# Optimization experiments

Hardware: AMD Instinct MI355X
Metric: run time of the kernel (lower is better)

The kernel has to match this reference:

```python
import jax, jax.numpy as jnp
import numpy as np

B, N_SRC, N_TGT = 2, 2048, 2048
DIM, HEADS, DIM_HEAD, DIM_ROT = 1024, 16, 64, 32
INNER = HEADS * DIM_HEAD
SCALE = DIM_HEAD ** -0.5


def rotate_every_two(x):
    # (..., d) with d even: pairs (x1, x2) -> (-x2, x1), interleaved
    x1 = x[..., ::2]
    x2 = x[..., 1::2]
    return jnp.stack((-x2, x1), axis=-1).reshape(x.shape)


def setup_inputs() -> dict:
    key = jax.random.key(0)
    ks = jax.random.split(key, 10)
    return {
        "src": jax.random.normal(ks[0], (B, N_SRC, DIM), jnp.float32),
        "sin_src": jax.random.uniform(ks[1], (B, N_SRC, DIM_ROT), jnp.float32, -1.0, 1.0),
        "cos_src": jax.random.uniform(ks[2], (B, N_SRC, DIM_ROT), jnp.float32, -1.0, 1.0),
        "tgt": jax.random.normal(ks[3], (B, N_TGT, DIM), jnp.float32),
        "sin_tgt": jax.random.uniform(ks[4], (B, N_TGT, DIM_ROT), jnp.float32, -1.0, 1.0),
        "cos_tgt": jax.random.uniform(ks[5], (B, N_TGT, DIM_ROT), jnp.float32, -1.0, 1.0),
        "wq": jax.random.normal(ks[6], (DIM, INNER), jnp.float32) / np.sqrt(DIM),
        "wkv": jax.random.normal(ks[7], (DIM, 2 * INNER), jnp.float32) / np.sqrt(DIM),
        "wout": jax.random.normal(ks[8], (INNER, DIM), jnp.float32) / np.sqrt(INNER),
        "bout": jnp.zeros((DIM,), jnp.float32),
    }


def reference(src, sin_src, cos_src, tgt, sin_tgt, cos_tgt, wq, wkv, wout, bout):
    b = src.shape[0]
    q = tgt @ wq                                  # (b, i, inner)
    k, v = jnp.split(src @ wkv, 2, axis=-1)       # (b, j, inner) each

    def split_heads(t):
        return t.reshape(b, t.shape[1], HEADS, DIM_HEAD).transpose(0, 2, 1, 3)

    q, k, v = map(split_heads, (q, k, v))          # (b, h, n, d)

    # rotary on leading DIM_ROT dims; pos embs broadcast across heads
    st, ct = sin_tgt[:, None], cos_tgt[:, None]    # (b, 1, i, dr)
    ss, cs = sin_src[:, None], cos_src[:, None]    # (b, 1, j, dr)
    q_rot, q_pass = q[..., :DIM_ROT], q[..., DIM_ROT:]
    k_rot, k_pass = k[..., :DIM_ROT], k[..., DIM_ROT:]
    q_rot = q_rot * ct + rotate_every_two(q_rot) * st
    k_rot = k_rot * cs + rotate_every_two(k_rot) * ss
    q = jnp.concatenate([q_rot, q_pass], axis=-1)
    k = jnp.concatenate([k_rot, k_pass], axis=-1)

    dots = jnp.einsum('bhid,bhjd->bhij', q, k) * SCALE
    attn = jax.nn.softmax(dots, axis=-1)
    out = jnp.einsum('bhij,bhjd->bhid', attn, v)
    out = out.transpose(0, 2, 1, 3).reshape(b, out.shape[2], INNER)
    return out @ wout + bout, attn
```

## Files before the change

### kernel.cpp

```cpp
#include <hip/hip_runtime.h>
#include <hip/hip_bf16.h>
#include <cstdint>
#include <cstddef>

#define NB 2
#define NSEQ 2048
#define NHEADS 16
#define HD 64
#define DMODEL 1024
#define SCALEF 0.125f

typedef __attribute__((ext_vector_type(4))) float f32x4;
typedef __attribute__((ext_vector_type(8))) short s16x8;

__device__ __forceinline__ unsigned short f2bf(float f) {
  union { float f; unsigned u; } v; v.f = f;
  unsigned u = v.u;
  return (unsigned short)((u + 0x7fffu + ((u >> 16) & 1u)) >> 16);
}

__global__ void k_convert(const float* __restrict__ in, unsigned short* __restrict__ out, int n4) {
  int i = blockIdx.x * blockDim.x + threadIdx.x;
  if (i >= n4) return;
  float4 v = ((const float4*)in)[i];
  ushort4 o;
  o.x = f2bf(v.x); o.y = f2bf(v.y); o.z = f2bf(v.z); o.w = f2bf(v.w);
  ((ushort4*)out)[i] = o;
}

__global__ void k_transpose(const float* __restrict__ w, unsigned short* __restrict__ wt, int K, int N) {
  __shared__ float t[64][65];
  int n0 = blockIdx.x * 64, k0 = blockIdx.y * 64;
  int c = threadIdx.x & 63, rb = threadIdx.x >> 6;
#pragma unroll
  for (int rr = 0; rr < 16; rr++) {
    int k = rb * 16 + rr;
    t[c][k] = w[(size_t)(k0 + k) * N + n0 + c];
  }
  __syncthreads();
#pragma unroll
  for (int rr = 0; rr < 16; rr++) {
    int n = rb * 16 + rr;
    wt[(size_t)(n0 + n) * K + k0 + c] = f2bf(t[n][c]);
  }
}

#define GLD16(gp, lp) __builtin_amdgcn_global_load_lds( \
    (const __attribute__((address_space(1))) unsigned int*)(gp), \
    (__attribute__((address_space(3))) unsigned int*)(lp), 16, 0, 0)

__global__ __launch_bounds__(256) void k_gemm(const unsigned short* __restrict__ A,
                                              const unsigned short* __restrict__ Bt,
                                              float* __restrict__ C,
                                              const float* __restrict__ bias,
                                              int M, int N, int K) {
  __shared__ unsigned short As[128 * 32];
  __shared__ unsigned short Bs[128 * 32];
  const int tid = threadIdx.x;
  const int lane = tid & 63, wid = tid >> 6;
  const int m0 = blockIdx.y * 128, n0 = blockIdx.x * 128;
  const int wr = wid >> 1, wc = wid & 1;
  const int lr = lane >> 2, l4 = lane & 3;
  const int lc = lane & 15, lg = lane >> 4;

  const unsigned short* pa0 = A + (size_t)(m0 + wid * 32 + lr) * K + l4 * 8;
  const unsigned short* pa1 = pa0 + (size_t)16 * K;
  const unsigned short* pb0 = Bt + (size_t)(n0 + wid * 32 + lr) * K + l4 * 8;
  const unsigned short* pb1 = pb0 + (size_t)16 * K;

  f32x4 acc[4][4] = {};

  for (int kt = 0; kt < K; kt += 32) {
    GLD16(pa0 + kt, &As[wid * 1024]);
    GLD16(pa1 + kt, &As[wid * 1024 + 512]);
    GLD16(pb0 + kt, &Bs[wid * 1024]);
    GLD16(pb1 + kt, &Bs[wid * 1024 + 512]);
    __syncthreads();
    s16x8 af[4], bfr[4];
#pragma unroll
    for (int m = 0; m < 4; m++)
      af[m] = *(const s16x8*)&As[(wr * 64 + m * 16 + lc) * 32 + lg * 8];
#pragma unroll
    for (int n = 0; n < 4; n++)
      bfr[n] = *(const s16x8*)&Bs[(wc * 64 + n * 16 + lc) * 32 + lg * 8];
    __builtin_amdgcn_s_setprio(1);
#pragma unroll
    for (int m = 0; m < 4; m++)
#pragma unroll
      for (int n = 0; n < 4; n++)
        acc[m][n] = __builtin_amdgcn_mfma_f32_16x16x32_bf16(af[m], bfr[n], acc[m][n], 0, 0, 0);
    __builtin_amdgcn_s_setprio(0);
    __syncthreads();
  }

  float bv[4] = {0.f, 0.f, 0.f, 0.f};
  if (bias) {
#pragma unroll
    for (int n = 0; n < 4; n++) bv[n] = bias[n0 + wc * 64 + n * 16 + lc];
  }
#pragma unroll
  for (int m = 0; m < 4; m++) {
#pragma unroll
    for (int n = 0; n < 4; n++) {
      int col = n0 + wc * 64 + n * 16 + lc;
#pragma unroll
      for (int r = 0; r < 4; r++) {
        int row = m0 + wr * 64 + m * 16 + lg * 4 + r;
        C[(size_t)row * N + col] = acc[m][n][r] + bv[n];
      }
    }
  }
}

__global__ void k_rope(const float* __restrict__ src, int row_stride,
                       const float* __restrict__ sinp, const float* __restrict__ cosp,
                       unsigned short* __restrict__ dst) {
  int tid = blockIdx.x * 256 + threadIdx.x;
  int p = tid & 31;
  int h = (tid >> 5) & 15;
  int i = (tid >> 9) & 2047;
  int b = tid >> 20;
  int d = p * 2;
  float2 x = *(const float2*)(src + (size_t)(b * NSEQ + i) * row_stride + h * HD + d);
  float o0, o1;
  if (p < 16) {
    size_t sc = (size_t)(b * NSEQ + i) * 32 + d;
    float2 cc = *(const float2*)(cosp + sc);
    float2 ss = *(const float2*)(sinp + sc);
    o0 = x.x * cc.x - x.y * ss.x;
    o1 = x.y * cc.y + x.x * ss.y;
  } else { o0 = x.x; o1 = x.y; }
  size_t off = ((size_t)(b * NHEADS + h) * NSEQ + i) * HD + d;
  unsigned pack = (unsigned)f2bf(o0) | ((unsigned)f2bf(o1) << 16);
  *(unsigned*)(dst + off) = pack;
}

__global__ void k_vtrans(const float* __restrict__ kv, unsigned short* __restrict__ vt) {
  __shared__ float t[64][65];
  int i0 = blockIdx.x * 64;
  int h = blockIdx.y, b = blockIdx.z;
  int c = threadIdx.x & 63, rb = threadIdx.x >> 6;
#pragma unroll
  for (int rr = 0; rr < 16; rr++) {
    int il = rb * 16 + rr;
    t[il][c] = kv[(size_t)(b * NSEQ + i0 + il) * 2048 + 1024 + h * HD + c];
  }
  __syncthreads();
#pragma unroll
  for (int rr = 0; rr < 16; rr++) {
    int dd = rb * 16 + rr;
    vt[((size_t)(b * NHEADS + h) * HD + dd) * NSEQ + i0 + c] = f2bf(t[c][dd]);
  }
}

#define SROWB 2056
__global__ __launch_bounds__(512, 4) void k_attn(const unsigned short* __restrict__ qh,
                                                 const unsigned short* __restrict__ kh,
                                                 const unsigned short* __restrict__ vt,
                                                 float* __restrict__ attn_g,
                                                 unsigned short* __restrict__ ctx) {
  __shared__ unsigned short Sbf[16 * SROWB];
  __shared__ float wred[8][16];
  __shared__ float rowmax_s[16];
  __shared__ float invr[16];
  float* part = (float*)Sbf;

  const int tid = threadIdx.x;
  const int lane = tid & 63, wid = tid >> 6;
  const int i0 = blockIdx.x * 16;
  const int h = blockIdx.y, b = blockIdx.z;
  const int lc = lane & 15, lg = lane >> 4;

  const unsigned short* qb = qh + ((size_t)(b * NHEADS + h) * NSEQ + i0) * HD;
  const unsigned short* kb = kh + (size_t)(b * NHEADS + h) * NSEQ * HD;
  const unsigned short* vb = vt + (size_t)(b * NHEADS + h) * HD * NSEQ;

  s16x8 aq0 = *(const s16x8*)&qb[lc * HD + lg * 8];
  s16x8 aq1 = *(const s16x8*)&qb[lc * HD + 32 + lg * 8];
  f32x4 sc[16];
  float mx[4] = {-1e30f, -1e30f, -1e30f, -1e30f};
#pragma unroll
  for (int jf = 0; jf < 16; jf++) {
    int j = wid * 256 + jf * 16;
    f32x4 acc = {};
    s16x8 bk0 = *(const s16x8*)&kb[(size_t)(j + lc) * HD + lg * 8];
    s16x8 bk1 = *(const s16x8*)&kb[(size_t)(j + lc) * HD + 32 + lg * 8];
    acc = __builtin_amdgcn_mfma_f32_16x16x32_bf16(aq0, bk0, acc, 0, 0, 0);
    acc = __builtin_amdgcn_mfma_f32_16x16x32_bf16(aq1, bk1, acc, 0, 0, 0);
#pragma unroll
    for (int r = 0; r < 4; r++) {
      float v = acc[r] * SCALEF;
      sc[jf][r] = v;
      mx[r] = fmaxf(mx[r], v);
    }
  }
#pragma unroll
  for (int off = 1; off <= 8; off <<= 1)
#pragma unroll
    for (int r = 0; r < 4; r++) mx[r] = fmaxf(mx[r], __shfl_xor(mx[r], off));
  if (lc == 0) {
#pragma unroll
    for (int r = 0; r < 4; r++) wred[wid][lg * 4 + r] = mx[r];
  }
  __syncthreads();
  if (tid < 16) {
    float m = -1e30f;
#pragma unroll
    for (int w = 0; w < 8; w++) m = fmaxf(m, wred[w][tid]);
    rowmax_s[tid] = m;
  }
  __syncthreads();

  float mrow[4], psum[4] = {0.f, 0.f, 0.f, 0.f};
#pragma unroll
  for (int r = 0; r < 4; r++) mrow[r] = rowmax_s[lg * 4 + r];
#pragma unroll
  for (int jf = 0; jf < 16; jf++) {
    int j = wid * 256 + jf * 16;
#pragma unroll
    for (int r = 0; r < 4; r++) {
      float e = __expf(sc[jf][r] - mrow[r]);
      sc[jf][r] = e;
      psum[r] += e;
      Sbf[(size_t)(lg * 4 + r) * SROWB + j + lc] = f2bf(e);
    }
  }
#pragma unroll
  for (int off = 1; off <= 8; off <<= 1)
#pragma unroll
    for (int r = 0; r < 4; r++) psum[r] += __shfl_xor(psum[r], off);
  if (lc == 0) {
#pragma unroll
    for (int r = 0; r < 4; r++) wred[wid][lg * 4 + r] = psum[r];
  }
  __syncthreads();
  if (tid < 16) {
    float s = 0.f;
#pragma unroll
    for (int w = 0; w < 8; w++) s += wred[w][tid];
    invr[tid] = 1.0f / s;
  }
  __syncthreads();

  float ivr[4];
#pragma unroll
  for (int r = 0; r < 4; r++) ivr[r] = invr[lg * 4 + r];
  {
    float* ab = attn_g + ((size_t)(b * NHEADS + h) * NSEQ + i0) * NSEQ + wid * 256 + lc;
#pragma unroll
    for (int jf = 0; jf < 16; jf++) {
#pragma unroll
      for (int r = 0; r < 4; r++)
        __builtin_nontemporal_store(sc[jf][r] * ivr[r],
                                    ab + (size_t)(lg * 4 + r) * NSEQ + jf * 16);
    }
  }

  f32x4 accd[4] = {};
#pragma unroll 2
  for (int jj = 0; jj < 8; jj++) {
    int jb = wid * 256 + jj * 32;
    s16x8 af = *(const s16x8*)&Sbf[(size_t)lc * SROWB + jb + lg * 8];
    __builtin_amdgcn_s_setprio(1);
#pragma unroll
    for (int f = 0; f < 4; f++) {
      s16x8 bv = *(const s16x8*)&vb[(size_t)(f * 16 + lc) * NSEQ + jb + lg * 8];
      accd[f] = __builtin_amdgcn_mfma_f32_16x16x32_bf16(af, bv, accd[f], 0, 0, 0);
    }
    __builtin_amdgcn_s_setprio(0);
  }
  __syncthreads();

  if (wid < 4) {
#pragma unroll
    for (int f = 0; f < 4; f++)
#pragma unroll
      for (int r = 0; r < 4; r++)
        part[((size_t)wid * 16 + lg * 4 + r) * 64 + f * 16 + lc] = accd[f][r];
  }
  __syncthreads();
  if (wid >= 4) {
#pragma unroll
    for (int f = 0; f < 4; f++)
#pragma unroll
      for (int r = 0; r < 4; r++)
        part[((size_t)(wid - 4) * 16 + lg * 4 + r) * 64 + f * 16 + lc] += accd[f][r];
  }
  __syncthreads();

  if (tid < 256) {
    const int oi = tid >> 4;
    const int d0 = (tid & 15) * 4;
    float4 p0 = *(float4*)&part[((size_t)0 * 16 + oi) * 64 + d0];
    float4 p1 = *(float4*)&part[((size_t)1 * 16 + oi) * 64 + d0];
    float4 p2 = *(float4*)&part[((size_t)2 * 16 + oi) * 64 + d0];
    float4 p3 = *(float4*)&part[((size_t)3 * 16 + oi) * 64 + d0];
    float iv = invr[oi];
    float4 tot;
    tot.x = (p0.x + p1.x + p2.x + p3.x) * iv;
    tot.y = (p0.y + p1.y + p2.y + p3.y) * iv;
    tot.z = (p0.z + p1.z + p2.z + p3.z) * iv;
    tot.w = (p0.w + p1.w + p2.w + p3.w) * iv;
    ushort4 o;
    o.x = f2bf(tot.x); o.y = f2bf(tot.y); o.z = f2bf(tot.z); o.w = f2bf(tot.w);
    *(ushort4*)&ctx[(size_t)(b * NSEQ + i0 + oi) * DMODEL + h * HD + d0] = o;
  }
}

extern "C" void kernel_launch(void* const* d_in, const int* in_sizes, int n_in,
                              void* d_out, int out_size, void* d_ws, size_t ws_size,
                              hipStream_t stream) {
  const float* src     = (const float*)d_in[0];
  const float* sin_src = (const float*)d_in[1];
  const float* cos_src = (const float*)d_in[2];
  const float* tgt     = (const float*)d_in[3];
  const float* sin_tgt = (const float*)d_in[4];
  const float* cos_tgt = (const float*)d_in[5];
  const float* wq      = (const float*)d_in[6];
  const float* wkv     = (const float*)d_in[7];
  const float* wout    = (const float*)d_in[8];
  const float* bout    = (const float*)d_in[9];

  if (ws_size < (size_t)109051904) return;

  uint8_t* w = (uint8_t*)d_ws;
  unsigned short* tgt_bf = (unsigned short*)(w + 0);
  unsigned short* src_bf = (unsigned short*)(w + 8388608);
  unsigned short* wq_t   = (unsigned short*)(w + 16777216);
  unsigned short* wkv_t  = (unsigned short*)(w + 18874368);
  unsigned short* wout_t = (unsigned short*)(w + 23068672);
  float*          q_ws   = (float*)(w + 25165824);
  float*          kv_ws  = (float*)(w + 41943040);
  unsigned short* qhb    = (unsigned short*)(w + 75497472);
  unsigned short* khb    = (unsigned short*)(w + 83886080);
  unsigned short* vtb    = (unsigned short*)(w + 92274688);
  unsigned short* ctx    = (unsigned short*)(w + 100663296);

  float* out_p  = (float*)d_out;
  float* attn_p = out_p + (size_t)NB * NSEQ * DMODEL;

  k_convert<<<4096, 256, 0, stream>>>(tgt, tgt_bf, 1048576);
  k_convert<<<4096, 256, 0, stream>>>(src, src_bf, 1048576);
  k_transpose<<<dim3(16, 16), 256, 0, stream>>>(wq,   wq_t,   1024, 1024);
  k_transpose<<<dim3(32, 16), 256, 0, stream>>>(wkv,  wkv_t,  1024, 2048);
  k_transpose<<<dim3(16, 16), 256, 0, stream>>>(wout, wout_t, 1024, 1024);

  k_gemm<<<dim3(8, 32),  256, 0, stream>>>(tgt_bf, wq_t,  q_ws,  nullptr, 4096, 1024, 1024);
  k_gemm<<<dim3(16, 32), 256, 0, stream>>>(src_bf, wkv_t, kv_ws, nullptr, 4096, 2048, 1024);

  k_rope<<<8192, 256, 0, stream>>>(q_ws, 1024, sin_tgt, cos_tgt, qhb);
  k_rope<<<8192, 256, 0, stream>>>(kv_ws, 2048, sin_src, cos_src, khb);
  k_vtrans<<<dim3(32, 16, 2), 256, 0, stream>>>(kv_ws, vtb);

  k_attn<<<dim3(128, 16, 2), 512, 0, stream>>>(qhb, khb, vtb, attn_p, ctx);

  k_gemm<<<dim3(8, 32), 256, 0, stream>>>(ctx, wout_t, out_p, bout, 4096, 1024, 1024);
}
```

Measured before the change: 412.8 us.

## Drop softmax max pass and write attention probs from bf16 LDS with vector stores

Removes the row-max reduction and its two barriers by exponentiating scaled scores directly, keeping no fp32 score registers. The normalized attention matrix is now rebuilt from the bf16 exponentials in LDS and written with 16-byte nontemporal row-contiguous stores instead of scattered scalar stores. This cuts register pressure, barriers and store transactions. In exchange the attn output loses precision (bf16-rounded) and overflow safety relies on scores being small.

```diff
diff --git a/kernel.cpp b/kernel.cpp
--- a/kernel.cpp
+++ b/kernel.cpp
@@ -17,6 +17,10 @@
   union { float f; unsigned u; } v; v.f = f;
   unsigned u = v.u;
   return (unsigned short)((u + 0x7fffu + ((u >> 16) & 1u)) >> 16);
+}
+__device__ __forceinline__ float bf2f(unsigned short s) {
+  union { unsigned u; float f; } v; v.u = ((unsigned)s) << 16;
+  return v.f;
 }
 
 __global__ void k_convert(const float* __restrict__ in, unsigned short* __restrict__ out, int n4) {
@@ -161,7 +165,6 @@
                                                  unsigned short* __restrict__ ctx) {
   __shared__ unsigned short Sbf[16 * SROWB];
   __shared__ float wred[8][16];
-  __shared__ float rowmax_s[16];
   __shared__ float invr[16];
   float* part = (float*)Sbf;
 
@@ -177,50 +180,20 @@
 
   s16x8 aq0 = *(const s16x8*)&qb[lc * HD + lg * 8];
   s16x8 aq1 = *(const s16x8*)&qb[lc * HD + 32 + lg * 8];
-  f32x4 sc[16];
-  float mx[4] = {-1e30f, -1e30f, -1e30f, -1e30f};
-#pragma unroll
+  float psum[4] = {0.f, 0.f, 0.f, 0.f};
+#pragma unroll 4
   for (int jf = 0; jf < 16; jf++) {
     int j = wid * 256 + jf * 16;
     f32x4 acc = {};
     s16x8 bk0 = *(const s16x8*)&kb[(size_t)(j + lc) * HD + lg * 8];
     s16x8 bk1 = *(const s16x8*)&kb[(size_t)(j + lc) * HD + 32 + lg * 8];
+    __builtin_amdgcn_s_setprio(1);
     acc = __builtin_amdgcn_mfma_f32_16x16x32_bf16(aq0, bk0, acc, 0, 0, 0);
     acc = __builtin_amdgcn_mfma_f32_16x16x32_bf16(aq1, bk1, acc, 0, 0, 0);
+    __builtin_amdgcn_s_setprio(0);
 #pragma unroll
     for (int r = 0; r < 4; r++) {
-      float v = acc[r] * SCALEF;
-      sc[jf][r] = v;
-      mx[r] = fmaxf(mx[r], v);
-    }
-  }
-#pragma unroll
-  for (int off = 1; off <= 8; off <<= 1)
-#pragma unroll
-    for (int r = 0; r < 4; r++) mx[r] = fmaxf(mx[r], __shfl_xor(mx[r], off));
-  if (lc == 0) {
-#pragma unroll
-    for (int r = 0; r < 4; r++) wred[wid][lg * 4 + r] = mx[r];
-  }
-  __syncthreads();
-  if (tid < 16) {
-    float m = -1e30f;
-#pragma unroll
-    for (int w = 0; w < 8; w++) m = fmaxf(m, wred[w][tid]);
-    rowmax_s[tid] = m;
-  }
-  __syncthreads();
-
-  float mrow[4], psum[4] = {0.f, 0.f, 0.f, 0.f};
-#pragma unroll
-  for (int r = 0; r < 4; r++) mrow[r] = rowmax_s[lg * 4 + r];
-#pragma unroll
-  for (int jf = 0; jf < 16; jf++) {
-    int j = wid * 256 + jf * 16;
-#pragma unroll
-    for (int r = 0; r < 4; r++) {
-      float e = __expf(sc[jf][r] - mrow[r]);
-      sc[jf][r] = e;
+      float e = __expf(acc[r] * SCALEF);
       psum[r] += e;
       Sbf[(size_t)(lg * 4 + r) * SROWB + j + lc] = f2bf(e);
     }
@@ -234,25 +207,32 @@
     for (int r = 0; r < 4; r++) wred[wid][lg * 4 + r] = psum[r];
   }
   __syncthreads();
-  if (tid < 16) {
-    float s = 0.f;
-#pragma unroll
-    for (int w = 0; w < 8; w++) s += wred[w][tid];
-    invr[tid] = 1.0f / s;
-  }
-  __syncthreads();
-
-  float ivr[4];
-#pragma unroll
-  for (int r = 0; r < 4; r++) ivr[r] = invr[lg * 4 + r];
+
+  const int row = tid >> 5;
+  const int c = tid & 31;
+  float tot = 0.f;
+#pragma unroll
+  for (int w = 0; w < 8; w++) tot += wred[w][row];
+  float inv = 1.0f / tot;
+  if (c == 0) invr[row] = inv;
+
   {
-    float* ab = attn_g + ((size_t)(b * NHEADS + h) * NSEQ + i0) * NSEQ + wid * 256 + lc;
-#pragma unroll
-    for (int jf = 0; jf < 16; jf++) {
-#pragma unroll
-      for (int r = 0; r < 4; r++)
-        __builtin_nontemporal_store(sc[jf][r] * ivr[r],
-                                    ab + (size_t)(lg * 4 + r) * NSEQ + jf * 16);
+    float* arow = attn_g + ((size_t)(b * NHEADS + h) * NSEQ + i0 + row) * NSEQ;
+#pragma unroll
+    for (int k = 0; k < 8; k++) {
+      int col = c * 8 + k * 256;
+      s16x8 ev = *(const s16x8*)&Sbf[(size_t)row * SROWB + col];
+      f32x4 f0, f1;
+      f0[0] = bf2f((unsigned short)ev[0]) * inv;
+      f0[1] = bf2f((unsigned short)ev[1]) * inv;
+      f0[2] = bf2f((unsigned short)ev[2]) * inv;
+      f0[3] = bf2f((unsigned short)ev[3]) * inv;
+      f1[0] = bf2f((unsigned short)ev[4]) * inv;
+      f1[1] = bf2f((unsigned short)ev[5]) * inv;
+      f1[2] = bf2f((unsigned short)ev[6]) * inv;
+      f1[3] = bf2f((unsigned short)ev[7]) * inv;
+      __builtin_nontemporal_store(f0, (f32x4*)&arow[col]);
+      __builtin_nontemporal_store(f1, (f32x4*)&arow[col + 4]);
     }
   }
 
```

Result: slower. 433.4 us (+5.0%).
